# Kernel tuning notes

Hardware: AMD Instinct MI355X
Metric: run time of the kernel (lower is better)

The kernel has to match this reference:

```python
import jax, jax.numpy as jnp
import numpy as np

D_MODEL = 1024
N_HEADS = 16
HEAD_DIM = 64
T = 4096
ROT = HEAD_DIM // 2          # 32 channels get rotary
PAIR = ROT // 2              # 16 cos/sin frequencies
EPS = 1e-6
SCALE = 0.12                 # constant attention scale (not 1/sqrt(d))
ROPE_BASE = 10000.0
VOCAB = 50257


def setup_inputs() -> dict:
    key = jax.random.key(0)
    k_x, k_qkv, k_o, k_tok = jax.random.split(key, 4)
    bound = 0.5 / np.sqrt(D_MODEL)
    x = jax.random.normal(k_x, (1, T, D_MODEL), dtype=jnp.float32)
    w_qkv = jax.random.uniform(k_qkv, (3 * D_MODEL, D_MODEL), jnp.float32, -bound, bound)
    # module uses zero_init for w_o; use small random so output is non-trivial
    w_o = jax.random.uniform(k_o, (D_MODEL, D_MODEL), jnp.float32, -bound, bound)
    q_norm_w = jnp.ones((HEAD_DIM,), jnp.float32)
    k_norm_w = jnp.ones((HEAD_DIM,), jnp.float32)
    tokens = jax.random.randint(k_tok, (1, T), 0, VOCAB, dtype=jnp.int64)
    pos = jnp.arange(T, dtype=jnp.int64)
    # RotaryCache: inv_freq over pair dims, cos/sin of t * inv_freq
    inv_freq = 1.0 / (ROPE_BASE ** (jnp.arange(PAIR, dtype=jnp.float32) / PAIR))
    freqs = jnp.arange(T, dtype=jnp.float32)[:, None] * inv_freq[None, :]  # [T, PAIR]
    return {
        "x": x, "tokens": tokens, "pos": pos,
        "w_qkv": w_qkv, "w_o": w_o,
        "q_norm_w": q_norm_w, "k_norm_w": k_norm_w,
        "cos": jnp.cos(freqs), "sin": jnp.sin(freqs),
        "window_tokens": 1024, "block_size": 128,
    }


def _rmsnorm(x, w):
    var = jnp.mean(x * x, axis=-1, keepdims=True)
    return x * jax.lax.rsqrt(var + EPS) * w


def reference(x, tokens, pos, w_qkv, w_o, q_norm_w, k_norm_w, cos, sin,
              window_tokens, block_size):
    B, Tq, C = x.shape
    H, Dh = N_HEADS, HEAD_DIM
    qkv = x @ w_qkv.T                                  # [B, T, 3C]
    q, k, v = jnp.split(qkv, 3, axis=-1)

    def to_bhtd(t):
        return t.reshape(B, Tq, H, Dh).transpose(0, 2, 1, 3)
    q, k, v = to_bhtd(q), to_bhtd(k), to_bhtd(v)

    q = _rmsnorm(q, q_norm_w)
    k = _rmsnorm(k, k_norm_w)

    # half-truncated RoPE: rotate first ROT channels pairwise (even/odd)
    c = cos[pos][None, None]                           # [1,1,T,PAIR]
    s = sin[pos][None, None]

    def rope_rotate(t):
        t1, t2 = t[..., :ROT], t[..., ROT:]
        even, odd = t1[..., 0::2], t1[..., 1::2]
        r_even = even * c - odd * s
        r_odd = even * s + odd * c
        t1r = jnp.stack([r_even, r_odd], axis=-1).reshape(t1.shape)
        return jnp.concatenate([t1r, t2], axis=-1)

    q = rope_rotate(q)
    k = rope_rotate(k)

    v = v * 0.5                                        # no value-embed branch

    scores = jnp.einsum('bhtd,bhsd->bhts', q, k) * SCALE
    idx = jnp.arange(Tq)
    diff = idx[:, None] - idx[None, :]
    allowed = (diff >= 0) & (diff < window_tokens)     # sliding causal window
    scores = jnp.where(allowed, scores, -jnp.inf)
    p = jax.nn.softmax(scores, axis=-1)
    out = jnp.einsum('bhts,bhsd->bhtd', p, v)
    out = out.transpose(0, 2, 1, 3).reshape(B, Tq, C)
    return out @ w_o.T
```

## Files before the change

kernel.cpp:

```cpp
#include <hip/hip_runtime.h>


typedef __bf16 bf16x8 __attribute__((ext_vector_type(8)));
typedef __bf16 bf16x2 __attribute__((ext_vector_type(2)));
typedef float f32x4 __attribute__((ext_vector_type(4)));
typedef unsigned short u16x8 __attribute__((ext_vector_type(8)));
typedef unsigned short u16x4 __attribute__((ext_vector_type(4)));

#define MFMA16(a, b, c) __builtin_amdgcn_mfma_f32_16x16x32_bf16((a), (b), (c), 0, 0, 0)

__device__ __forceinline__ unsigned short f2bf(float f) {
    unsigned int u = __float_as_uint(f);
    u += 0x7fffu + ((u >> 16) & 1u);
    return (unsigned short)(u >> 16);
}
__device__ __forceinline__ float bf2f(unsigned short h) {
    return __uint_as_float(((unsigned int)h) << 16);
}
__device__ __forceinline__ unsigned int pk2bf(float a, float b) {
#if __has_builtin(__builtin_amdgcn_cvt_pk_bf16_f32)
    bf16x2 v = __builtin_amdgcn_cvt_pk_bf16_f32(a, b);
    return __builtin_bit_cast(unsigned int, v);
#else
    return (unsigned int)f2bf(a) | ((unsigned int)f2bf(b) << 16);
#endif
}
__device__ __forceinline__ float fexp2(float x) {
#if __has_builtin(__builtin_amdgcn_exp2f)
    return __builtin_amdgcn_exp2f(x);
#else
    return exp2f(x);
#endif
}

__device__ __forceinline__ void gl_lds16(const void* g, void* l) {
    typedef __attribute__((address_space(1))) unsigned int GU;
    typedef __attribute__((address_space(3))) unsigned int LU;
    __builtin_amdgcn_global_load_lds((GU*)(unsigned long long)g,
                                     (LU*)(unsigned int)(unsigned long long)l,
                                     16, 0, 0);
}

__global__ void cvt3_kernel(const float* __restrict__ x,
                            const float* __restrict__ wqkv,
                            const float* __restrict__ wo,
                            unsigned short* __restrict__ xb,
                            unsigned short* __restrict__ wqkvb,
                            unsigned short* __restrict__ wob) {
    int i = blockIdx.x * 256 + threadIdx.x;
    const float* src;
    unsigned short* dst;
    int off;
    if (i < 1048576) { src = x; dst = xb; off = i; }
    else if (i < 1835008) { src = wqkv; dst = wqkvb; off = i - 1048576; }
    else { src = wo; dst = wob; off = i - 1835008; }
    float4 f = ((const float4*)src)[off];
    u16x4 o;
    o[0] = f2bf(f.x); o[1] = f2bf(f.y); o[2] = f2bf(f.z); o[3] = f2bf(f.w);
    ((u16x4*)dst)[off] = o;
}

#define TBS 72
__global__ __launch_bounds__(256, 6) void gemm_qkv(
    const unsigned short* __restrict__ A,
    const unsigned short* __restrict__ Bt,
    const float* __restrict__ cosb, const float* __restrict__ sinb,
    const float* __restrict__ qw, const float* __restrict__ kw,
    unsigned short* __restrict__ Qb,
    unsigned short* __restrict__ Kb,
    unsigned short* __restrict__ Vt)
{
    __shared__ unsigned short smem[12288];
    unsigned short* As0 = smem;
    unsigned short* As1 = smem + 2048;
    unsigned short* Bs0 = smem + 4096;
    unsigned short* Bs1 = smem + 8192;

    const int tid = threadIdx.x;
    const int wave = tid >> 6, lane = tid & 63;
    const int quad = lane >> 4, l16 = lane & 15;
    const int m0 = blockIdx.x * 64, n0 = blockIdx.y * 128;
    const int wm = (wave >> 1) * 32, wn = (wave & 1) * 64;

    f32x4 acc[2][4];
#pragma unroll
    for (int i = 0; i < 2; ++i)
#pragma unroll
        for (int j = 0; j < 4; ++j) acc[i][j] = (f32x4){0.f, 0.f, 0.f, 0.f};

    const int lrow = lane >> 2;
    const int lcol = ((lane & 3) ^ ((lane >> 3) & 3)) * 8;
    const int csw  = (quad ^ ((l16 >> 1) & 3)) * 8;

    for (int k0 = 0; k0 < 1024; k0 += 64) {
        {
            const unsigned short* ab = A + (size_t)(m0 + wave * 16 + lrow) * 1024 + k0 + lcol;
            gl_lds16(ab,      &As0[wave * 512]);
            gl_lds16(ab + 32, &As1[wave * 512]);
        }
#pragma unroll
        for (int i = 0; i < 2; ++i) {
            const int c = wave * 2 + i;
            const unsigned short* bb = Bt + (size_t)(n0 + c * 16 + lrow) * 1024 + k0 + lcol;
            gl_lds16(bb,      &Bs0[c * 512]);
            gl_lds16(bb + 32, &Bs1[c * 512]);
        }
        __syncthreads();
        {
            bf16x8 af[2], bfr[4];
#pragma unroll
            for (int mt = 0; mt < 2; ++mt)
                af[mt] = *(const bf16x8*)&As0[(wm + mt * 16 + l16) * 32 + csw];
#pragma unroll
            for (int nt = 0; nt < 4; ++nt)
                bfr[nt] = *(const bf16x8*)&Bs0[(wn + nt * 16 + l16) * 32 + csw];
#pragma unroll
            for (int mt = 0; mt < 2; ++mt)
#pragma unroll
                for (int nt = 0; nt < 4; ++nt)
                    acc[mt][nt] = MFMA16(af[mt], bfr[nt], acc[mt][nt]);
        }
        {
            bf16x8 af[2], bfr[4];
#pragma unroll
            for (int mt = 0; mt < 2; ++mt)
                af[mt] = *(const bf16x8*)&As1[(wm + mt * 16 + l16) * 32 + csw];
#pragma unroll
            for (int nt = 0; nt < 4; ++nt)
                bfr[nt] = *(const bf16x8*)&Bs1[(wn + nt * 16 + l16) * 32 + csw];
#pragma unroll
            for (int mt = 0; mt < 2; ++mt)
#pragma unroll
                for (int nt = 0; nt < 4; ++nt)
                    acc[mt][nt] = MFMA16(af[mt], bfr[nt], acc[mt][nt]);
        }
        __syncthreads();
    }

    unsigned short* tbw = smem + wave * 1152;
    const int region = blockIdx.y >> 3;
    const int h = ((blockIdx.y & 7) << 1) + (wave & 1);

    if (region < 2) {
        const float* wgt = region ? kw : qw;
        unsigned short* dst = region ? Kb : Qb;
        const float post = region ? 1.f : 0.17312340490667046f;
        float w[4];
#pragma unroll
        for (int nt = 0; nt < 4; ++nt) w[nt] = wgt[nt * 16 + l16] * post;
#pragma unroll
        for (int mt = 0; mt < 2; ++mt) {
#pragma unroll
            for (int r = 0; r < 4; ++r) {
                const int row = m0 + wm + mt * 16 + quad * 4 + r;
                float ss = 0.f;
#pragma unroll
                for (int nt = 0; nt < 4; ++nt)
                    ss += acc[mt][nt][r] * acc[mt][nt][r];
                ss += __shfl_xor(ss, 1); ss += __shfl_xor(ss, 2);
                ss += __shfl_xor(ss, 4); ss += __shfl_xor(ss, 8);
                const float rn = rsqrtf(ss * (1.f / 64.f) + 1e-6f);
                float val[4];
#pragma unroll
                for (int nt = 0; nt < 4; ++nt)
                    val[nt] = acc[mt][nt][r] * rn * w[nt];
#pragma unroll
                for (int nt = 0; nt < 2; ++nt) {
                    const float prt = __shfl_xor(val[nt], 1);
                    const int p = nt * 8 + (l16 >> 1);
                    const float c = cosb[row * 16 + p];
                    const float s = sinb[row * 16 + p];
                    val[nt] = (l16 & 1) ? (prt * s + val[nt] * c)
                                        : (val[nt] * c - prt * s);
                }
#pragma unroll
                for (int nt = 0; nt < 4; ++nt)
                    tbw[(quad * 4 + r) * TBS + nt * 16 + l16] = f2bf(val[nt]);
            }
            const int t = lane >> 2, dcol = (lane & 3) * 16;
            u16x8 v0 = *(const u16x8*)&tbw[t * TBS + dcol];
            u16x8 v1 = *(const u16x8*)&tbw[t * TBS + dcol + 8];
            const size_t ob = ((size_t)h * 4096 + (m0 + wm + mt * 16 + t)) * 64 + dcol;
            *(u16x8*)&dst[ob] = v0;
            *(u16x8*)&dst[ob + 8] = v1;
        }
    } else {
#pragma unroll
        for (int mt = 0; mt < 2; ++mt) {
#pragma unroll
            for (int nt = 0; nt < 4; ++nt)
#pragma unroll
                for (int r = 0; r < 4; ++r)
                    tbw[(nt * 16 + l16) * 16 + quad * 4 + r] =
                        f2bf(acc[mt][nt][r] * 0.5f);
            u16x8 v0 = *(const u16x8*)&tbw[lane * 16];
            u16x8 v1 = *(const u16x8*)&tbw[lane * 16 + 8];
            const size_t vo = ((size_t)h * 64 + lane) * 4096 + m0 + wm + mt * 16;
            *(u16x8*)&Vt[vo] = v0;
            *(u16x8*)&Vt[vo + 8] = v1;
        }
    }
}

#define PSTR 72

template <int MODE>
__device__ __forceinline__ void attn_compute(
    int s0, int tq, int quad, int l16, int csw,
    const unsigned short* Ks0, const unsigned short* Ks1,
    const unsigned short* Vs0, const unsigned short* Vs1,
    unsigned short* Pw, const bf16x8 qf0, const bf16x8 qf1,
    f32x4 (&o)[4], float& lsum)
{
#pragma unroll
    for (int i = 0; i < 4; ++i) {
        const bf16x8 kf0 = *(const bf16x8*)&Ks0[(i * 16 + l16) * 32 + csw];
        const bf16x8 kf1 = *(const bf16x8*)&Ks1[(i * 16 + l16) * 32 + csw];
        f32x4 z = (f32x4){0.f, 0.f, 0.f, 0.f};
        z = MFMA16(kf0, qf0, z);
        z = MFMA16(kf1, qf1, z);
        float p[4];
#pragma unroll
        for (int r = 0; r < 4; ++r) {
            float e = fexp2(z[r]);
            if (MODE == 1) {
                const int s = s0 + i * 16 + quad * 4 + r;
                e = ((tq - s) < 1024) ? e : 0.f;
            }
            if (MODE == 2) {
                const int s = s0 + i * 16 + quad * 4 + r;
                e = (s <= tq) ? e : 0.f;
            }
            p[r] = e;
            lsum += e;
        }
        uint2 pk;
        pk.x = pk2bf(p[0], p[1]);
        pk.y = pk2bf(p[2], p[3]);
        *(uint2*)&Pw[l16 * PSTR + i * 16 + quad * 4] = pk;
    }
    const bf16x8 pf0 = *(const bf16x8*)&Pw[l16 * PSTR + quad * 8];
    const bf16x8 pf1 = *(const bf16x8*)&Pw[l16 * PSTR + 32 + quad * 8];
#pragma unroll
    for (int dt = 0; dt < 4; ++dt) {
        const bf16x8 vf0 = *(const bf16x8*)&Vs0[(dt * 16 + l16) * 32 + csw];
        const bf16x8 vf1 = *(const bf16x8*)&Vs1[(dt * 16 + l16) * 32 + csw];
        o[dt] = MFMA16(pf0, vf0, o[dt]);
        o[dt] = MFMA16(pf1, vf1, o[dt]);
    }
}

__global__ __launch_bounds__(256) void attn_kernel(
    const unsigned short* __restrict__ Qb,
    const unsigned short* __restrict__ Kb,
    const unsigned short* __restrict__ Vt,
    unsigned short* __restrict__ att)
{
    __shared__ unsigned short Ks0[2][2048], Ks1[2][2048];
    __shared__ unsigned short Vs0[2][2048], Vs1[2][2048];
    __shared__ unsigned short P[4][16 * PSTR];

    const int bid = blockIdx.x;
    const int h = ((bid & 7) << 1) | ((bid >> 3) & 1);
    const int t0 = (63 - (bid >> 4)) * 64;

    const int tid = threadIdx.x;
    const int wave = tid >> 6, lane = tid & 63;
    const int quad = lane >> 4, l16 = lane & 15;
    const int qt0 = t0 + wave * 16;
    const int tq = qt0 + l16;
    const int krow = tid >> 2;
    const int kcol = ((tid & 3) ^ ((tid >> 3) & 3)) * 8;
    const int csw  = (quad ^ ((l16 >> 1) & 3)) * 8;

    const unsigned short* Qh = Qb + (size_t)h * 4096 * 64;
    const unsigned short* Kh = Kb + (size_t)h * 4096 * 64;
    const unsigned short* Vh = Vt + (size_t)h * 64 * 4096;

    const bf16x8 qf0 = *(const bf16x8*)&Qh[(qt0 + l16) * 64 + quad * 8];
    const bf16x8 qf1 = *(const bf16x8*)&Qh[(qt0 + l16) * 64 + 32 + quad * 8];

    f32x4 o[4];
#pragma unroll
    for (int dt = 0; dt < 4; ++dt) o[dt] = (f32x4){0.f, 0.f, 0.f, 0.f};
    float lsum = 0.f;
    unsigned short* Pw = P[wave];

    auto stage = [&](int b, int s0) {
        const unsigned short* kb = Kh + (size_t)(s0 + krow) * 64 + kcol;
        const unsigned short* vb = Vh + (size_t)krow * 4096 + s0 + kcol;
        gl_lds16(kb,      &Ks0[b][wave * 512]);
        gl_lds16(kb + 32, &Ks1[b][wave * 512]);
        gl_lds16(vb,      &Vs0[b][wave * 512]);
        gl_lds16(vb + 32, &Vs1[b][wave * 512]);
    };

    int s0 = (t0 >= 1024) ? (t0 - 1024) : 0;
    stage(0, s0);
    __syncthreads();
    int buf = 0;

    if (t0 >= 1024) {
        stage(1, s0 + 64);
        attn_compute<1>(s0, tq, quad, l16, csw, Ks0[0], Ks1[0], Vs0[0], Vs1[0],
                        Pw, qf0, qf1, o, lsum);
        __syncthreads();
        buf = 1; s0 += 64;
    }
    for (; s0 < t0; s0 += 64) {
        stage(buf ^ 1, s0 + 64);
        attn_compute<0>(s0, tq, quad, l16, csw, Ks0[buf], Ks1[buf], Vs0[buf],
                        Vs1[buf], Pw, qf0, qf1, o, lsum);
        __syncthreads();
        buf ^= 1;
    }
    attn_compute<2>(t0, tq, quad, l16, csw, Ks0[buf], Ks1[buf], Vs0[buf],
                    Vs1[buf], Pw, qf0, qf1, o, lsum);

    lsum += __shfl_xor(lsum, 16);
    lsum += __shfl_xor(lsum, 32);
    float lr[4];
#pragma unroll
    for (int r = 0; r < 4; ++r) lr[r] = 1.f / __shfl(lsum, quad * 4 + r);
#pragma unroll
    for (int dt = 0; dt < 4; ++dt)
#pragma unroll
        for (int r = 0; r < 4; ++r)
            att[(size_t)(qt0 + quad * 4 + r) * 1024 + h * 64 + dt * 16 + l16] =
                f2bf(o[dt][r] * lr[r]);
}

__global__ __launch_bounds__(256) void gemm_out(
    const unsigned short* __restrict__ A,
    const unsigned short* __restrict__ Bt,
    float* __restrict__ C)
{
    __shared__ unsigned short As0[2][2048], As1[2][2048];
    __shared__ unsigned short Bs0[2][4096], Bs1[2][4096];
    const int tid = threadIdx.x;
    const int wave = tid >> 6, lane = tid & 63;
    const int quad = lane >> 4, l16 = lane & 15;
    const int m0 = blockIdx.x * 64, n0 = blockIdx.y * 128;
    const int wm = (wave >> 1) * 32, wn = (wave & 1) * 64;
    const int lrow = lane >> 2;
    const int lcol = ((lane & 3) ^ ((lane >> 3) & 3)) * 8;
    const int csw  = (quad ^ ((l16 >> 1) & 3)) * 8;

    f32x4 acc[2][4];
#pragma unroll
    for (int i = 0; i < 2; ++i)
#pragma unroll
        for (int j = 0; j < 4; ++j) acc[i][j] = (f32x4){0.f, 0.f, 0.f, 0.f};

    auto stage = [&](int buf, int k0) {
        const unsigned short* ab = A + (size_t)(m0 + wave * 16 + lrow) * 1024 + k0 + lcol;
        gl_lds16(ab,      &As0[buf][wave * 512]);
        gl_lds16(ab + 32, &As1[buf][wave * 512]);
#pragma unroll
        for (int i = 0; i < 2; ++i) {
            const int c = wave * 2 + i;
            const unsigned short* bb = Bt + (size_t)(n0 + c * 16 + lrow) * 1024 + k0 + lcol;
            gl_lds16(bb,      &Bs0[buf][c * 512]);
            gl_lds16(bb + 32, &Bs1[buf][c * 512]);
        }
    };

    stage(0, 0);
    __syncthreads();
    int buf = 0;
    for (int k0 = 0; k0 < 1024; k0 += 64) {
        if (k0 + 64 < 1024) stage(buf ^ 1, k0 + 64);
        {
            bf16x8 af[2], bfr[4];
#pragma unroll
            for (int mt = 0; mt < 2; ++mt)
                af[mt] = *(const bf16x8*)&As0[buf][(wm + mt * 16 + l16) * 32 + csw];
#pragma unroll
            for (int nt = 0; nt < 4; ++nt)
                bfr[nt] = *(const bf16x8*)&Bs0[buf][(wn + nt * 16 + l16) * 32 + csw];
#pragma unroll
            for (int mt = 0; mt < 2; ++mt)
#pragma unroll
                for (int nt = 0; nt < 4; ++nt)
                    acc[mt][nt] = MFMA16(af[mt], bfr[nt], acc[mt][nt]);
        }
        {
            bf16x8 af[2], bfr[4];
#pragma unroll
            for (int mt = 0; mt < 2; ++mt)
                af[mt] = *(const bf16x8*)&As1[buf][(wm + mt * 16 + l16) * 32 + csw];
#pragma unroll
            for (int nt = 0; nt < 4; ++nt)
                bfr[nt] = *(const bf16x8*)&Bs1[buf][(wn + nt * 16 + l16) * 32 + csw];
#pragma unroll
            for (int mt = 0; mt < 2; ++mt)
#pragma unroll
                for (int nt = 0; nt < 4; ++nt)
                    acc[mt][nt] = MFMA16(af[mt], bfr[nt], acc[mt][nt]);
        }
        __syncthreads();
        buf ^= 1;
    }
#pragma unroll
    for (int mt = 0; mt < 2; ++mt)
#pragma unroll
        for (int nt = 0; nt < 4; ++nt)
#pragma unroll
            for (int r = 0; r < 4; ++r) {
                const int row = m0 + wm + mt * 16 + quad * 4 + r;
                const int col = n0 + wn + nt * 16 + l16;
                C[(size_t)row * 1024 + col] = acc[mt][nt][r];
            }
}

extern "C" void kernel_launch(void* const* d_in, const int* in_sizes, int n_in,
                              void* d_out, int out_size, void* d_ws, size_t ws_size,
                              hipStream_t stream) {
    const float* x    = (const float*)d_in[0];
    const float* wqkv = (const float*)d_in[3];
    const float* wo   = (const float*)d_in[4];
    const float* qw   = (const float*)d_in[5];
    const float* kw   = (const float*)d_in[6];
    const float* cosb = (const float*)d_in[7];
    const float* sinb = (const float*)d_in[8];

    char* ws = (char*)d_ws;
    if (ws_size < (size_t)48 * 1024 * 1024) return;
    unsigned short* xb    = (unsigned short*)(ws + ((size_t)0 << 20));
    unsigned short* wqkvb = (unsigned short*)(ws + ((size_t)8 << 20));
    unsigned short* wob   = (unsigned short*)(ws + ((size_t)14 << 20));
    unsigned short* Qb    = (unsigned short*)(ws + ((size_t)16 << 20));
    unsigned short* Kb    = (unsigned short*)(ws + ((size_t)24 << 20));
    unsigned short* Vt    = (unsigned short*)(ws + ((size_t)32 << 20));
    unsigned short* attb  = (unsigned short*)(ws + ((size_t)40 << 20));

    cvt3_kernel<<<8192, 256, 0, stream>>>(x, wqkv, wo, xb, wqkvb, wob);

    gemm_qkv<<<dim3(64, 24), 256, 0, stream>>>(xb, wqkvb, cosb, sinb, qw, kw,
                                               Qb, Kb, Vt);

    attn_kernel<<<1024, 256, 0, stream>>>(Qb, Kb, Vt, attb);

    gemm_out<<<dim3(64, 8), 256, 0, stream>>>(attb, wob, (float*)d_out);
}
```

Before: 179.5 us.

## Enlarge QKV GEMM tile to 128x128 and attention block to 128 queries

The QKV projection GEMM now computes a 128x128 output tile per block, with each wave holding 4x4 MFMA accumulators. This halves the grid and raises operand reuse per byte loaded into shared memory. The attention kernel now uses 512-thread blocks covering 128 query rows that share each staged K/V tile. Half the waves load K and half load V, and a unified loop skips or masks key tiles per wave using a single unsigned window check. The cost is more registers and LDS per block, lower occupancy, and a wasted tile iteration for some waves at the diagonal and window edges.

```diff
diff --git a/kernel.cpp b/kernel.cpp
--- a/kernel.cpp
+++ b/kernel.cpp
@@ -61,7 +61,7 @@
 }
 
 #define TBS 72
-__global__ __launch_bounds__(256, 6) void gemm_qkv(
+__global__ __launch_bounds__(256, 3) void gemm_qkv(
     const unsigned short* __restrict__ A,
     const unsigned short* __restrict__ Bt,
     const float* __restrict__ cosb, const float* __restrict__ sinb,
@@ -70,21 +70,21 @@
     unsigned short* __restrict__ Kb,
     unsigned short* __restrict__ Vt)
 {
-    __shared__ unsigned short smem[12288];
+    __shared__ unsigned short smem[16384];
     unsigned short* As0 = smem;
-    unsigned short* As1 = smem + 2048;
-    unsigned short* Bs0 = smem + 4096;
-    unsigned short* Bs1 = smem + 8192;
+    unsigned short* As1 = smem + 4096;
+    unsigned short* Bs0 = smem + 8192;
+    unsigned short* Bs1 = smem + 12288;
 
     const int tid = threadIdx.x;
     const int wave = tid >> 6, lane = tid & 63;
     const int quad = lane >> 4, l16 = lane & 15;
-    const int m0 = blockIdx.x * 64, n0 = blockIdx.y * 128;
-    const int wm = (wave >> 1) * 32, wn = (wave & 1) * 64;
-
-    f32x4 acc[2][4];
-#pragma unroll
-    for (int i = 0; i < 2; ++i)
+    const int m0 = blockIdx.x * 128, n0 = blockIdx.y * 128;
+    const int wm = (wave >> 1) * 64, wn = (wave & 1) * 64;
+
+    f32x4 acc[4][4];
+#pragma unroll
+    for (int i = 0; i < 4; ++i)
 #pragma unroll
         for (int j = 0; j < 4; ++j) acc[i][j] = (f32x4){0.f, 0.f, 0.f, 0.f};
 
@@ -95,41 +95,41 @@
     for (int k0 = 0; k0 < 1024; k0 += 64) {
         {
             const unsigned short* ab = A + (size_t)(m0 + wave * 16 + lrow) * 1024 + k0 + lcol;
-            gl_lds16(ab,      &As0[wave * 512]);
-            gl_lds16(ab + 32, &As1[wave * 512]);
-        }
-#pragma unroll
-        for (int i = 0; i < 2; ++i) {
-            const int c = wave * 2 + i;
-            const unsigned short* bb = Bt + (size_t)(n0 + c * 16 + lrow) * 1024 + k0 + lcol;
-            gl_lds16(bb,      &Bs0[c * 512]);
-            gl_lds16(bb + 32, &Bs1[c * 512]);
+            gl_lds16(ab,              &As0[wave * 512]);
+            gl_lds16(ab + 32,         &As1[wave * 512]);
+            gl_lds16(ab + 65536,      &As0[2048 + wave * 512]);
+            gl_lds16(ab + 65536 + 32, &As1[2048 + wave * 512]);
+            const unsigned short* bb = Bt + (size_t)(n0 + wave * 16 + lrow) * 1024 + k0 + lcol;
+            gl_lds16(bb,              &Bs0[wave * 512]);
+            gl_lds16(bb + 32,         &Bs1[wave * 512]);
+            gl_lds16(bb + 65536,      &Bs0[2048 + wave * 512]);
+            gl_lds16(bb + 65536 + 32, &Bs1[2048 + wave * 512]);
         }
         __syncthreads();
         {
-            bf16x8 af[2], bfr[4];
-#pragma unroll
-            for (int mt = 0; mt < 2; ++mt)
+            bf16x8 af[4], bfr[4];
+#pragma unroll
+            for (int mt = 0; mt < 4; ++mt)
                 af[mt] = *(const bf16x8*)&As0[(wm + mt * 16 + l16) * 32 + csw];
 #pragma unroll
             for (int nt = 0; nt < 4; ++nt)
                 bfr[nt] = *(const bf16x8*)&Bs0[(wn + nt * 16 + l16) * 32 + csw];
 #pragma unroll
-            for (int mt = 0; mt < 2; ++mt)
+            for (int mt = 0; mt < 4; ++mt)
 #pragma unroll
                 for (int nt = 0; nt < 4; ++nt)
                     acc[mt][nt] = MFMA16(af[mt], bfr[nt], acc[mt][nt]);
         }
         {
-            bf16x8 af[2], bfr[4];
-#pragma unroll
-            for (int mt = 0; mt < 2; ++mt)
+            bf16x8 af[4], bfr[4];
+#pragma unroll
+            for (int mt = 0; mt < 4; ++mt)
                 af[mt] = *(const bf16x8*)&As1[(wm + mt * 16 + l16) * 32 + csw];
 #pragma unroll
             for (int nt = 0; nt < 4; ++nt)
                 bfr[nt] = *(const bf16x8*)&Bs1[(wn + nt * 16 + l16) * 32 + csw];
 #pragma unroll
-            for (int mt = 0; mt < 2; ++mt)
+            for (int mt = 0; mt < 4; ++mt)
 #pragma unroll
                 for (int nt = 0; nt < 4; ++nt)
                     acc[mt][nt] = MFMA16(af[mt], bfr[nt], acc[mt][nt]);
@@ -149,7 +149,7 @@
 #pragma unroll
         for (int nt = 0; nt < 4; ++nt) w[nt] = wgt[nt * 16 + l16] * post;
 #pragma unroll
-        for (int mt = 0; mt < 2; ++mt) {
+        for (int mt = 0; mt < 4; ++mt) {
 #pragma unroll
             for (int r = 0; r < 4; ++r) {
                 const int row = m0 + wm + mt * 16 + quad * 4 + r;
@@ -186,7 +186,7 @@
         }
     } else {
 #pragma unroll
-        for (int mt = 0; mt < 2; ++mt) {
+        for (int mt = 0; mt < 4; ++mt) {
 #pragma unroll
             for (int nt = 0; nt < 4; ++nt)
 #pragma unroll
@@ -204,7 +204,7 @@
 
 #define PSTR 72
 
-template <int MODE>
+template <int MASK>
 __device__ __forceinline__ void attn_compute(
     int s0, int tq, int quad, int l16, int csw,
     const unsigned short* Ks0, const unsigned short* Ks1,
@@ -223,13 +223,9 @@
 #pragma unroll
         for (int r = 0; r < 4; ++r) {
             float e = fexp2(z[r]);
-            if (MODE == 1) {
+            if (MASK) {
                 const int s = s0 + i * 16 + quad * 4 + r;
-                e = ((tq - s) < 1024) ? e : 0.f;
-            }
-            if (MODE == 2) {
-                const int s = s0 + i * 16 + quad * 4 + r;
-                e = (s <= tq) ? e : 0.f;
+                e = ((unsigned)(tq - s) < 1024u) ? e : 0.f;
             }
             p[r] = e;
             lsum += e;
@@ -250,7 +246,7 @@
     }
 }
 
-__global__ __launch_bounds__(256) void attn_kernel(
+__global__ __launch_bounds__(512, 4) void attn_kernel(
     const unsigned short* __restrict__ Qb,
     const unsigned short* __restrict__ Kb,
     const unsigned short* __restrict__ Vt,
@@ -258,19 +254,19 @@
 {
     __shared__ unsigned short Ks0[2][2048], Ks1[2][2048];
     __shared__ unsigned short Vs0[2][2048], Vs1[2][2048];
-    __shared__ unsigned short P[4][16 * PSTR];
+    __shared__ unsigned short P[8][16 * PSTR];
 
     const int bid = blockIdx.x;
     const int h = ((bid & 7) << 1) | ((bid >> 3) & 1);
-    const int t0 = (63 - (bid >> 4)) * 64;
+    const int t0 = (31 - (bid >> 4)) * 128;
 
     const int tid = threadIdx.x;
     const int wave = tid >> 6, lane = tid & 63;
     const int quad = lane >> 4, l16 = lane & 15;
     const int qt0 = t0 + wave * 16;
     const int tq = qt0 + l16;
-    const int krow = tid >> 2;
-    const int kcol = ((tid & 3) ^ ((tid >> 3) & 3)) * 8;
+    const int srow = (tid & 255) >> 2;
+    const int scol = ((tid & 3) ^ ((tid >> 3) & 3)) * 8;
     const int csw  = (quad ^ ((l16 >> 1) & 3)) * 8;
 
     const unsigned short* Qh = Qb + (size_t)h * 4096 * 64;
@@ -287,35 +283,37 @@
     unsigned short* Pw = P[wave];
 
     auto stage = [&](int b, int s0) {
-        const unsigned short* kb = Kh + (size_t)(s0 + krow) * 64 + kcol;
-        const unsigned short* vb = Vh + (size_t)krow * 4096 + s0 + kcol;
-        gl_lds16(kb,      &Ks0[b][wave * 512]);
-        gl_lds16(kb + 32, &Ks1[b][wave * 512]);
-        gl_lds16(vb,      &Vs0[b][wave * 512]);
-        gl_lds16(vb + 32, &Vs1[b][wave * 512]);
+        if (wave < 4) {
+            const unsigned short* kb = Kh + (size_t)(s0 + srow) * 64 + scol;
+            gl_lds16(kb,      &Ks0[b][wave * 512]);
+            gl_lds16(kb + 32, &Ks1[b][wave * 512]);
+        } else {
+            const unsigned short* vb = Vh + (size_t)srow * 4096 + s0 + scol;
+            gl_lds16(vb,      &Vs0[b][(wave - 4) * 512]);
+            gl_lds16(vb + 32, &Vs1[b][(wave - 4) * 512]);
+        }
     };
 
-    int s0 = (t0 >= 1024) ? (t0 - 1024) : 0;
-    stage(0, s0);
+    const int s_lo = (t0 >= 1024) ? (t0 - 1024) : 0;
+    const int s_hi = t0 + 64;
+    stage(0, s_lo);
     __syncthreads();
     int buf = 0;
-
-    if (t0 >= 1024) {
-        stage(1, s0 + 64);
-        attn_compute<1>(s0, tq, quad, l16, csw, Ks0[0], Ks1[0], Vs0[0], Vs1[0],
-                        Pw, qf0, qf1, o, lsum);
-        __syncthreads();
-        buf = 1; s0 += 64;
-    }
-    for (; s0 < t0; s0 += 64) {
-        stage(buf ^ 1, s0 + 64);
-        attn_compute<0>(s0, tq, quad, l16, csw, Ks0[buf], Ks1[buf], Vs0[buf],
-                        Vs1[buf], Pw, qf0, qf1, o, lsum);
+    for (int s0 = s_lo; s0 <= s_hi; s0 += 64) {
+        if (s0 < s_hi) stage(buf ^ 1, s0 + 64);
+        const bool dead = (s0 > qt0 + 15) || (s0 + 63 < qt0 - 1023);
+        if (!dead) {
+            const bool clean = (s0 + 63 <= qt0) && (s0 >= qt0 - 1008);
+            if (clean)
+                attn_compute<0>(s0, tq, quad, l16, csw, Ks0[buf], Ks1[buf],
+                                Vs0[buf], Vs1[buf], Pw, qf0, qf1, o, lsum);
+            else
+                attn_compute<1>(s0, tq, quad, l16, csw, Ks0[buf], Ks1[buf],
+                                Vs0[buf], Vs1[buf], Pw, qf0, qf1, o, lsum);
+        }
         __syncthreads();
         buf ^= 1;
     }
-    attn_compute<2>(t0, tq, quad, l16, csw, Ks0[buf], Ks1[buf], Vs0[buf],
-                    Vs1[buf], Pw, qf0, qf1, o, lsum);
 
     lsum += __shfl_xor(lsum, 16);
     lsum += __shfl_xor(lsum, 32);
@@ -436,10 +434,10 @@
 
     cvt3_kernel<<<8192, 256, 0, stream>>>(x, wqkv, wo, xb, wqkvb, wob);
 
-    gemm_qkv<<<dim3(64, 24), 256, 0, stream>>>(xb, wqkvb, cosb, sinb, qw, kw,
+    gemm_qkv<<<dim3(32, 24), 256, 0, stream>>>(xb, wqkvb, cosb, sinb, qw, kw,
                                                Qb, Kb, Vt);
 
-    attn_kernel<<<1024, 256, 0, stream>>>(Qb, Kb, Vt, attb);
+    attn_kernel<<<512, 512, 0, stream>>>(Qb, Kb, Vt, attb);
 
     gemm_out<<<dim3(64, 8), 256, 0, stream>>>(attb, wob, (float*)d_out);
 }
```

Result: no change. 177.9 us (-0.9%).
